# Optimization experiments

Hardware: AMD Instinct MI355X
Metric: run time of the kernel (lower is better)

The kernel has to match this reference:

```python
import jax, jax.numpy as jnp
import numpy as np

H = 10   # GRU hidden size
L = 10   # num layers
E = 400  # embedding dim
V = 100000
T, B = 84, 96


def gru_layer(x, w_ih, w_hh, b_ih, b_hh, reverse):
    # x: (T, B, in_dim); w_ih: (3H, in_dim); w_hh: (3H, H)
    xp = jnp.einsum('tbi,gi->tbg', x, w_ih) + b_ih  # (T, B, 3H)
    if reverse:
        xp = xp[::-1]

    def step(h, xt):
        gh = h @ w_hh.T + b_hh
        xr, xz, xn = jnp.split(xt, 3, axis=-1)
        hr, hz, hn = jnp.split(gh, 3, axis=-1)
        r = jax.nn.sigmoid(xr + hr)
        z = jax.nn.sigmoid(xz + hz)
        n = jnp.tanh(xn + r * hn)
        h_new = (1.0 - z) * n + z * h
        return h_new, h_new

    h0 = jnp.zeros((x.shape[1], H), x.dtype)
    _, ys = jax.lax.scan(step, h0, xp)
    if reverse:
        ys = ys[::-1]
    return ys  # (T, B, H)


def setup_inputs():
    key = jax.random.key(0)
    ks = jax.random.split(key, 12)
    s = 0.05
    return {
        'x': jax.random.randint(ks[0], (T, B), 0, V),
        'emb': jax.random.normal(ks[1], (V, E), jnp.float32) * 0.1,
        'w_ih0': jax.random.normal(ks[2], (2, 3 * H, E), jnp.float32) * s,
        'w_hh0': jax.random.normal(ks[3], (2, 3 * H, H), jnp.float32) * s,
        'b_ih0': jax.random.normal(ks[4], (2, 3 * H), jnp.float32) * s,
        'b_hh0': jax.random.normal(ks[5], (2, 3 * H), jnp.float32) * s,
        'w_ih': jax.random.normal(ks[6], (L - 1, 2, 3 * H, 2 * H), jnp.float32) * s,
        'w_hh': jax.random.normal(ks[7], (L - 1, 2, 3 * H, H), jnp.float32) * s,
        'b_ih': jax.random.normal(ks[8], (L - 1, 2, 3 * H), jnp.float32) * s,
        'b_hh': jax.random.normal(ks[9], (L - 1, 2, 3 * H), jnp.float32) * s,
        'lin_w': jax.random.normal(ks[10], (19, 336), jnp.float32) * s,
        'lin_b': jax.random.normal(ks[11], (19,), jnp.float32) * s,
    }


def reference(x, emb, w_ih0, w_hh0, b_ih0, b_hh0, w_ih, w_hh, b_ih, b_hh, lin_w, lin_b):
    out = emb[x]  # (T, B, 400)
    for l in range(L):
        if l == 0:
            wi, wh, bi, bh = w_ih0, w_hh0, b_ih0, b_hh0
        else:
            wi, wh, bi, bh = w_ih[l - 1], w_hh[l - 1], b_ih[l - 1], b_hh[l - 1]
        fwd = gru_layer(out, wi[0], wh[0], bi[0], bh[0], False)
        bwd = gru_layer(out, wi[1], wh[1], bi[1], bh[1], True)
        out = jnp.concatenate([fwd, bwd], axis=-1)  # (T, B, 20)
        # dropout p=0.2 between layers is disabled (eval-mode reference)
    # AvgPool2d(3)/MaxPool2d(3) on 3D input pool over (batch, feature) dims
    trimmed = out[:, : (B // 3) * 3, :18].reshape(T, B // 3, 3, 6, 3)
    avg = trimmed.mean(axis=(2, 4))  # (T, B//3, 6)
    mx = trimmed.max(axis=(2, 4))    # (T, B//3, 6)
    cat = jnp.concatenate([avg, mx], axis=2)  # (T, B//3, 12)
    flat = cat.reshape(-1, 336)  # (96, 336)
    # dropout p=0.2 disabled (eval-mode reference)
    return jax.nn.sigmoid(flat @ lin_w.T + lin_b)
```

## Files before the change

### kernel.cpp

```cpp
#include <hip/hip_runtime.h>
#include <math.h>

#define TT 84
#define BB 96
#define GB 6
#define NG 16
#define NTOK (TT*BB)
#define RW4 6

#define S_RZ (-1.4426950408889634f)
#define S_N  (-2.8853900817779268f)

__device__ __forceinline__ float frcp(float x)  { return __builtin_amdgcn_rcpf(x); }
__device__ __forceinline__ float fexp2(float x) { return __builtin_amdgcn_exp2f(x); }

__global__ __launch_bounds__(256) void proj0_kernel(
    const int* __restrict__ x, const float* __restrict__ emb,
    const float* __restrict__ wih0, const float* __restrict__ bih0,
    float* __restrict__ xp, unsigned int* __restrict__ bar)
{
    if (blockIdx.x == 0 && threadIdx.x == 0) bar[0] = 0u;
    __shared__ float4 xrow[32][100];
    const int tok0 = blockIdx.x * 32;
    for (int u = threadIdx.x; u < 32*100; u += 256) {
        int tk = u / 100, i4 = u % 100;
        int row = x[tok0 + tk];
        xrow[tk][i4] = ((const float4*)emb)[row*100 + i4];
    }
    __syncthreads();
    const int g64 = threadIdx.x & 63;
    const int q   = threadIdx.x >> 6;
    if (g64 >= 60) return;
    const int dir = g64 / 30, gg = g64 % 30;
    const float sc = (gg < 20) ? S_RZ : S_N;
    const float bias = bih0[dir*30 + gg];
    float acc[8];
    #pragma unroll
    for (int c = 0; c < 8; ++c) acc[c] = bias;
    const float4* w4 = ((const float4*)wih0) + (dir*30 + gg)*100;
    for (int i4 = 0; i4 < 100; ++i4) {
        float4 w = w4[i4];
        #pragma unroll
        for (int c = 0; c < 8; ++c) {
            float4 xv = xrow[q*8 + c][i4];
            acc[c] += w.x*xv.x + w.y*xv.y + w.z*xv.z + w.w*xv.w;
        }
    }
    #pragma unroll
    for (int c = 0; c < 8; ++c) {
        int tok = tok0 + q*8 + c;
        int t = tok / BB, b = tok % BB;
        xp[((size_t)((dir*TT + t)*BB + b))*30 + gg] = acc[c]*sc;
    }
}

__device__ __forceinline__ float gru_cell10(
    float xr, float xz, float xn, const float* h,
    const float* wr, const float* wz, const float* wn,
    float bhr, float bhz, float bhn, float& hown)
{
    float hr0 = fmaf(wr[0], h[0], bhr), hr1 = wr[1]*h[1];
    float hz0 = fmaf(wz[0], h[0], bhz), hz1 = wz[1]*h[1];
    float hn0 = fmaf(wn[0], h[0], bhn), hn1 = wn[1]*h[1];
    hr0 = fmaf(wr[2], h[2], hr0); hr1 = fmaf(wr[3], h[3], hr1);
    hz0 = fmaf(wz[2], h[2], hz0); hz1 = fmaf(wz[3], h[3], hz1);
    hn0 = fmaf(wn[2], h[2], hn0); hn1 = fmaf(wn[3], h[3], hn1);
    hr0 = fmaf(wr[4], h[4], hr0); hr1 = fmaf(wr[5], h[5], hr1);
    hz0 = fmaf(wz[4], h[4], hz0); hz1 = fmaf(wz[5], h[5], hz1);
    hn0 = fmaf(wn[4], h[4], hn0); hn1 = fmaf(wn[5], h[5], hn1);
    hr0 = fmaf(wr[6], h[6], hr0); hr1 = fmaf(wr[7], h[7], hr1);
    hz0 = fmaf(wz[6], h[6], hz0); hz1 = fmaf(wz[7], h[7], hz1);
    hn0 = fmaf(wn[6], h[6], hn0); hn1 = fmaf(wn[7], h[7], hn1);
    hr0 = fmaf(wr[8], h[8], hr0); hr1 = fmaf(wr[9], h[9], hr1);
    hz0 = fmaf(wz[8], h[8], hz0); hz1 = fmaf(wz[9], h[9], hz1);
    hn0 = fmaf(wn[8], h[8], hn0); hn1 = fmaf(wn[9], h[9], hn1);
    float r = frcp(1.f + fexp2(xr + hr0 + hr1));
    float z = frcp(1.f + fexp2(xz + hz0 + hz1));
    float an = fmaf(r, hn0 + hn1, xn);
    float n  = fmaf(2.f, frcp(1.f + fexp2(an)), -1.f);
    float hnew = n + z*(hown - n);
    hown = hnew;
    return hnew;
}

__device__ __forceinline__ void proj20(
    const float4* A, const float* wpr, const float* wpz, const float* wpn,
    float bir, float biz, float bin, float& xr, float& xz, float& xn)
{
    float a[24];
    #pragma unroll
    for (int q = 0; q < 6; ++q) {
        a[4*q]=A[q].x; a[4*q+1]=A[q].y; a[4*q+2]=A[q].z; a[4*q+3]=A[q].w;
    }
    xr = bir; xz = biz; xn = bin;
    #pragma unroll
    for (int c = 0; c < 20; ++c) {
        float av = a[c + (c >= 10 ? 2 : 0)];
        xr = fmaf(wpr[c], av, xr); xz = fmaf(wpz[c], av, xz); xn = fmaf(wpn[c], av, xn);
    }
}

__device__ __forceinline__ void scan_layer(
    const float* __restrict__ xb,
    const float* __restrict__ wh, const float* __restrict__ bh3,
    float4* __restrict__ act4, float* __restrict__ actG, bool last,
    int bl, int j, bool act_ln, int b, int dir, int dt, int t0)
{
    float wr[10], wz[10], wn[10];
    {
        const float2* p0 = (const float2*)(wh + j*10);
        const float2* p1 = (const float2*)(wh + (10+j)*10);
        const float2* p2 = (const float2*)(wh + (20+j)*10);
        #pragma unroll
        for (int q = 0; q < 5; ++q) {
            float2 a = p0[q]; wr[2*q]=a.x*S_RZ; wr[2*q+1]=a.y*S_RZ;
            float2 c = p1[q]; wz[2*q]=c.x*S_RZ; wz[2*q+1]=c.y*S_RZ;
            float2 d = p2[q]; wn[2*q]=d.x*S_N;  wn[2*q+1]=d.y*S_N;
        }
    }
    const float bhr = bh3[j]*S_RZ, bhz = bh3[10+j]*S_RZ, bhn = bh3[20+j]*S_N;

    const int base = bl*10;
    float h[10];
    #pragma unroll
    for (int k = 0; k < 10; ++k) h[k] = 0.f;
    float hown = 0.f;
    int t = t0;
    float xr0 = xb[(size_t)(t0*BB + b)*30 + j];
    float xz0 = xb[(size_t)(t0*BB + b)*30 + 10 + j];
    float xn0 = xb[(size_t)(t0*BB + b)*30 + 20 + j];
    const int t1 = t0 + dt;
    float xr1 = xb[(size_t)(t1*BB + b)*30 + j];
    float xz1 = xb[(size_t)(t1*BB + b)*30 + 10 + j];
    float xn1 = xb[(size_t)(t1*BB + b)*30 + 20 + j];

    #pragma unroll 1
    for (int s = 0; s < TT; ++s) {
        float hnew = gru_cell10(xr0, xz0, xn0, h, wr, wz, wn, bhr, bhz, bhn, hown);
        #pragma unroll
        for (int k = 0; k < 10; ++k) h[k] = __shfl(hnew, base + k, 64);
        if (!last) {
            ((float*)&act4[(t*GB + bl)*RW4])[dir*12 + j] = hnew;
        } else if (act_ln) {
            actG[(size_t)(t*BB + b)*20 + dir*10 + j] = hnew;
        }
        int tp = t + 2*dt; tp = tp < 0 ? 0 : (tp > TT-1 ? TT-1 : tp);
        xr0 = xr1; xz0 = xz1; xn0 = xn1;
        const float* px = xb + (size_t)(tp*BB + b)*30;
        xr1 = px[j]; xz1 = px[10 + j]; xn1 = px[20 + j];
        t += dt;
    }
}

__global__ __launch_bounds__(256, 1) void mega_kernel(
    float* __restrict__ xp,
    const float* __restrict__ whh0, const float* __restrict__ bhh0,
    const float* __restrict__ wih,  const float* __restrict__ bih,
    const float* __restrict__ whh,  const float* __restrict__ bhh,
    const float* __restrict__ lin_w, const float* __restrict__ lin_b,
    float* __restrict__ actG, unsigned int* __restrict__ bar,
    float* __restrict__ out)
{
    __shared__ float4 act4[TT*GB*RW4];

    const int tid  = threadIdx.x;
    const int grp  = blockIdx.x;

    const int dir  = (tid >> 6) & 1;
    const int lane = tid & 63;
    int bl = lane / 10; if (bl > 5) bl = 5;
    int j  = lane - bl*10; if (j > 9) j = 9;
    const bool act_ln = (lane < 60);
    const int b  = grp*GB + bl;
    const int dt = dir ? -1 : 1;
    const int t0 = dir ? TT-1 : 0;

    const int half = tid / 120;
    const int prr  = tid % 120;
    const int dp   = prr / 60;
    const int prr2 = prr % 60;
    const int blp  = prr2 / 10;
    const int jp   = prr2 % 10;

    #pragma unroll 1
    for (int l = 0; l < 10; ++l) {
        if (tid < 128) {
            const float* wh  = (l == 0) ? (whh0 + dir*300)
                                        : (whh + (size_t)((l-1)*2 + dir)*300);
            const float* bh3 = (l == 0) ? (bhh0 + dir*30)
                                        : (bhh + (size_t)((l-1)*2 + dir)*30);
            scan_layer(xp + (size_t)dir*TT*BB*30, wh, bh3, act4, actG, (l == 9),
                       bl, j, act_ln, b, dir, dt, t0);
        }
        __syncthreads();
        if (l < 9) {
            if (tid < 240) {
                const float* wi = wih + (size_t)(l*2 + dp)*600;
                const float* bi = bih + (size_t)(l*2 + dp)*30;
                float wpr[20], wpz[20], wpn[20];
                {
                    const float4* p0 = (const float4*)(wi + jp*20);
                    const float4* p1 = (const float4*)(wi + (10+jp)*20);
                    const float4* p2 = (const float4*)(wi + (20+jp)*20);
                    #pragma unroll
                    for (int q = 0; q < 5; ++q) {
                        float4 a = p0[q]; wpr[4*q]=a.x*S_RZ; wpr[4*q+1]=a.y*S_RZ; wpr[4*q+2]=a.z*S_RZ; wpr[4*q+3]=a.w*S_RZ;
                        float4 c = p1[q]; wpz[4*q]=c.x*S_RZ; wpz[4*q+1]=c.y*S_RZ; wpz[4*q+2]=c.z*S_RZ; wpz[4*q+3]=c.w*S_RZ;
                        float4 d = p2[q]; wpn[4*q]=d.x*S_N;  wpn[4*q+1]=d.y*S_N;  wpn[4*q+2]=d.z*S_N;  wpn[4*q+3]=d.w*S_N;
                    }
                }
                const float bir = bi[jp]*S_RZ, biz = bi[10+jp]*S_RZ, bin = bi[20+jp]*S_N;
                const int bg = grp*GB + blp;
                #pragma unroll 1
                for (int t = half*(TT/2); t < (half+1)*(TT/2); ++t) {
                    float xr, xz, xn;
                    proj20(&act4[(t*GB + blp)*RW4], wpr, wpz, wpn, bir, biz, bin, xr, xz, xn);
                    float* px = xp + ((size_t)(dp*TT + t)*BB + bg)*30;
                    px[jp] = xr; px[10+jp] = xz; px[20+jp] = xn;
                }
            }
            __syncthreads();
        }
    }

    __threadfence();
    __syncthreads();
    if (tid == 0) {
        __hip_atomic_fetch_add(bar, 1u, __ATOMIC_ACQ_REL, __HIP_MEMORY_SCOPE_AGENT);
        while (__hip_atomic_load(bar, __ATOMIC_ACQUIRE, __HIP_MEMORY_SCOPE_AGENT) < (unsigned)NG)
            __builtin_amdgcn_s_sleep(1);
    }
    __syncthreads();
    __threadfence();

    float* feat = (float*)act4;
    for (int u = tid; u < GB*336; u += 256) {
        int q = u / 336, v = u % 336;
        int r = grp*GB + q;
        int qq = v / 12, f = v % 12;
        int pair = r*28 + qq;
        int t = pair / 32, bb = pair % 32;
        int jj = (f < 6) ? f : f - 6;
        float acc = (f < 6) ? 0.f : -1e30f;
        #pragma unroll
        for (int i = 0; i < 3; ++i) {
            #pragma unroll
            for (int kk = 0; kk < 3; ++kk) {
                float vv = actG[(size_t)(t*BB + bb*3 + i)*20 + jj*3 + kk];
                if (f < 6) acc += vv; else acc = fmaxf(acc, vv);
            }
        }
        feat[u] = (f < 6) ? acc*(1.f/9.f) : acc;
    }
    __syncthreads();
    if (tid < GB*19) {
        int q = tid / 19, o = tid % 19;
        int r = grp*GB + q;
        float acc = lin_b[o];
        const float* wrow = lin_w + o*336;
        const float* frow = feat + q*336;
        for (int v = 0; v < 336; ++v) acc = fmaf(frow[v], wrow[v], acc);
        out[r*19 + o] = frcp(1.f + __expf(-acc));
    }
}

extern "C" void kernel_launch(void* const* d_in, const int* in_sizes, int n_in,
                              void* d_out, int out_size, void* d_ws, size_t ws_size,
                              hipStream_t stream)
{
    const int*   x     = (const int*)  d_in[0];
    const float* emb   = (const float*)d_in[1];
    const float* wih0  = (const float*)d_in[2];
    const float* whh0  = (const float*)d_in[3];
    const float* bih0  = (const float*)d_in[4];
    const float* bhh0  = (const float*)d_in[5];
    const float* wih   = (const float*)d_in[6];
    const float* whh   = (const float*)d_in[7];
    const float* bih   = (const float*)d_in[8];
    const float* bhh   = (const float*)d_in[9];
    const float* lin_w = (const float*)d_in[10];
    const float* lin_b = (const float*)d_in[11];
    float* out = (float*)d_out;

    float* xp0  = (float*)d_ws;
    float* actG = xp0 + (size_t)2*NTOK*30;
    unsigned int* bar = (unsigned int*)(actG + (size_t)NTOK*20);

    proj0_kernel<<<252, 256, 0, stream>>>(x, emb, wih0, bih0, xp0, bar);
    mega_kernel<<<NG, 256, 0, stream>>>(xp0, whh0, bhh0, wih, bih, whh, bhh,
                                        lin_w, lin_b, actG, bar, out);
}
```

Measured before the change: 532.7 us.

## Remap GRU scan to 16-lane rows with DPP rotate broadcast of hidden state

The recurrent scan is reorganised so each sequence occupies a 16-lane DPP row, and three wavefronts now hold all 12 sequences where two did before. The ten per-step __shfl broadcasts of the hidden state are replaced by row_ror DPP moves, with the recurrent weights pre-rotated and zero-padded to 16 entries. Padding lanes write to a trash slot in shared memory instead of branching. The aim is to cut cross-lane latency on the serial critical path, at the cost of 16-wide dot products (more FMAs per step) and extra registers.

```diff
diff --git a/kernel.cpp b/kernel.cpp
--- a/kernel.cpp
+++ b/kernel.cpp
@@ -13,6 +13,12 @@
 
 __device__ __forceinline__ float frcp(float x)  { return __builtin_amdgcn_rcpf(x); }
 __device__ __forceinline__ float fexp2(float x) { return __builtin_amdgcn_exp2f(x); }
+
+template<int M>
+__device__ __forceinline__ float dpp_ror(float v) {
+    return __int_as_float(__builtin_amdgcn_update_dpp(
+        0, __float_as_int(v), 0x120 + M, 0xf, 0xf, true));
+}
 
 __global__ __launch_bounds__(256) void proj0_kernel(
     const int* __restrict__ x, const float* __restrict__ emb,
@@ -54,35 +60,6 @@
     }
 }
 
-__device__ __forceinline__ float gru_cell10(
-    float xr, float xz, float xn, const float* h,
-    const float* wr, const float* wz, const float* wn,
-    float bhr, float bhz, float bhn, float& hown)
-{
-    float hr0 = fmaf(wr[0], h[0], bhr), hr1 = wr[1]*h[1];
-    float hz0 = fmaf(wz[0], h[0], bhz), hz1 = wz[1]*h[1];
-    float hn0 = fmaf(wn[0], h[0], bhn), hn1 = wn[1]*h[1];
-    hr0 = fmaf(wr[2], h[2], hr0); hr1 = fmaf(wr[3], h[3], hr1);
-    hz0 = fmaf(wz[2], h[2], hz0); hz1 = fmaf(wz[3], h[3], hz1);
-    hn0 = fmaf(wn[2], h[2], hn0); hn1 = fmaf(wn[3], h[3], hn1);
-    hr0 = fmaf(wr[4], h[4], hr0); hr1 = fmaf(wr[5], h[5], hr1);
-    hz0 = fmaf(wz[4], h[4], hz0); hz1 = fmaf(wz[5], h[5], hz1);
-    hn0 = fmaf(wn[4], h[4], hn0); hn1 = fmaf(wn[5], h[5], hn1);
-    hr0 = fmaf(wr[6], h[6], hr0); hr1 = fmaf(wr[7], h[7], hr1);
-    hz0 = fmaf(wz[6], h[6], hz0); hz1 = fmaf(wz[7], h[7], hz1);
-    hn0 = fmaf(wn[6], h[6], hn0); hn1 = fmaf(wn[7], h[7], hn1);
-    hr0 = fmaf(wr[8], h[8], hr0); hr1 = fmaf(wr[9], h[9], hr1);
-    hz0 = fmaf(wz[8], h[8], hz0); hz1 = fmaf(wz[9], h[9], hz1);
-    hn0 = fmaf(wn[8], h[8], hn0); hn1 = fmaf(wn[9], h[9], hn1);
-    float r = frcp(1.f + fexp2(xr + hr0 + hr1));
-    float z = frcp(1.f + fexp2(xz + hz0 + hz1));
-    float an = fmaf(r, hn0 + hn1, xn);
-    float n  = fmaf(2.f, frcp(1.f + fexp2(an)), -1.f);
-    float hnew = n + z*(hown - n);
-    hown = hnew;
-    return hnew;
-}
-
 __device__ __forceinline__ void proj20(
     const float4* A, const float* wpr, const float* wpz, const float* wpn,
     float bir, float biz, float bin, float& xr, float& xz, float& xn)
@@ -100,54 +77,86 @@
     }
 }
 
-__device__ __forceinline__ void scan_layer(
+template<bool LAST>
+__device__ __forceinline__ void scan16(
     const float* __restrict__ xb,
     const float* __restrict__ wh, const float* __restrict__ bh3,
-    float4* __restrict__ act4, float* __restrict__ actG, bool last,
-    int bl, int j, bool act_ln, int b, int dir, int dt, int t0)
-{
-    float wr[10], wz[10], wn[10];
-    {
-        const float2* p0 = (const float2*)(wh + j*10);
-        const float2* p1 = (const float2*)(wh + (10+j)*10);
-        const float2* p2 = (const float2*)(wh + (20+j)*10);
-        #pragma unroll
-        for (int q = 0; q < 5; ++q) {
-            float2 a = p0[q]; wr[2*q]=a.x*S_RZ; wr[2*q+1]=a.y*S_RZ;
-            float2 c = p1[q]; wz[2*q]=c.x*S_RZ; wz[2*q+1]=c.y*S_RZ;
-            float2 d = p2[q]; wn[2*q]=d.x*S_N;  wn[2*q+1]=d.y*S_N;
-        }
-    }
-    const float bhr = bh3[j]*S_RZ, bhz = bh3[10+j]*S_RZ, bhn = bh3[20+j]*S_N;
-
-    const int base = bl*10;
-    float h[10];
-    #pragma unroll
-    for (int k = 0; k < 10; ++k) h[k] = 0.f;
-    float hown = 0.f;
+    float* __restrict__ actF, float* __restrict__ actG,
+    int j, int jw, int bl, int dir, int b, int dt, int t0,
+    bool realw, int trashIdx)
+{
+    float wsr[16], wsz[16], wsn[16];
+    #pragma unroll
+    for (int m = 0; m < 16; ++m) {
+        int k  = (j - m) & 15;
+        int kc = (k < 10) ? k : 9;
+        float zr = (k < 10) ? S_RZ : 0.f;
+        float zn = (k < 10) ? S_N  : 0.f;
+        wsr[m] = wh[       jw*10 + kc] * zr;
+        wsz[m] = wh[100 +  jw*10 + kc] * zr;
+        wsn[m] = wh[200 +  jw*10 + kc] * zn;
+    }
+    const float bhr = bh3[jw]*S_RZ, bhz = bh3[10+jw]*S_RZ, bhn = bh3[20+jw]*S_N;
+
+    float h[16];
+    #pragma unroll
+    for (int m = 0; m < 16; ++m) h[m] = 0.f;
+
     int t = t0;
-    float xr0 = xb[(size_t)(t0*BB + b)*30 + j];
-    float xz0 = xb[(size_t)(t0*BB + b)*30 + 10 + j];
-    float xn0 = xb[(size_t)(t0*BB + b)*30 + 20 + j];
+    const size_t lbo = (size_t)b*30 + jw;
+    float xr0 = xb[(size_t)t0*(BB*30) + lbo];
+    float xz0 = xb[(size_t)t0*(BB*30) + lbo + 10];
+    float xn0 = xb[(size_t)t0*(BB*30) + lbo + 20];
     const int t1 = t0 + dt;
-    float xr1 = xb[(size_t)(t1*BB + b)*30 + j];
-    float xz1 = xb[(size_t)(t1*BB + b)*30 + 10 + j];
-    float xn1 = xb[(size_t)(t1*BB + b)*30 + 20 + j];
+    float xr1 = xb[(size_t)t1*(BB*30) + lbo];
+    float xz1 = xb[(size_t)t1*(BB*30) + lbo + 10];
+    float xn1 = xb[(size_t)t1*(BB*30) + lbo + 20];
 
     #pragma unroll 1
     for (int s = 0; s < TT; ++s) {
-        float hnew = gru_cell10(xr0, xz0, xn0, h, wr, wz, wn, bhr, bhz, bhn, hown);
+        float ar0 = fmaf(wsr[0], h[0], xr0 + bhr), ar1 = wsr[1]*h[1];
+        float az0 = fmaf(wsz[0], h[0], xz0 + bhz), az1 = wsz[1]*h[1];
+        float an0 = fmaf(wsn[0], h[0], bhn),       an1 = wsn[1]*h[1];
         #pragma unroll
-        for (int k = 0; k < 10; ++k) h[k] = __shfl(hnew, base + k, 64);
-        if (!last) {
-            ((float*)&act4[(t*GB + bl)*RW4])[dir*12 + j] = hnew;
-        } else if (act_ln) {
-            actG[(size_t)(t*BB + b)*20 + dir*10 + j] = hnew;
-        }
+        for (int m = 2; m < 16; m += 2) {
+            ar0 = fmaf(wsr[m], h[m], ar0); ar1 = fmaf(wsr[m+1], h[m+1], ar1);
+            az0 = fmaf(wsz[m], h[m], az0); az1 = fmaf(wsz[m+1], h[m+1], az1);
+            an0 = fmaf(wsn[m], h[m], an0); an1 = fmaf(wsn[m+1], h[m+1], an1);
+        }
+        float r  = frcp(1.f + fexp2(ar0 + ar1));
+        float z  = frcp(1.f + fexp2(az0 + az1));
+        float an = fmaf(r, an0 + an1, xn0);
+        float n  = fmaf(2.f, frcp(1.f + fexp2(an)), -1.f);
+        float hown = h[0];
+        float hnew = n + z*(hown - n);
+
+        int widx = realw ? ((t*GB + bl)*24 + dir*12 + j) : trashIdx;
+        actF[widx] = hnew;
+        if (LAST) {
+            if (realw) actG[(size_t)(t*BB + b)*20 + dir*10 + j] = hnew;
+        }
+
+        h[0]  = hnew;
+        h[1]  = dpp_ror<1>(hnew);
+        h[2]  = dpp_ror<2>(hnew);
+        h[3]  = dpp_ror<3>(hnew);
+        h[4]  = dpp_ror<4>(hnew);
+        h[5]  = dpp_ror<5>(hnew);
+        h[6]  = dpp_ror<6>(hnew);
+        h[7]  = dpp_ror<7>(hnew);
+        h[8]  = dpp_ror<8>(hnew);
+        h[9]  = dpp_ror<9>(hnew);
+        h[10] = dpp_ror<10>(hnew);
+        h[11] = dpp_ror<11>(hnew);
+        h[12] = dpp_ror<12>(hnew);
+        h[13] = dpp_ror<13>(hnew);
+        h[14] = dpp_ror<14>(hnew);
+        h[15] = dpp_ror<15>(hnew);
+
         int tp = t + 2*dt; tp = tp < 0 ? 0 : (tp > TT-1 ? TT-1 : tp);
         xr0 = xr1; xz0 = xz1; xn0 = xn1;
-        const float* px = xb + (size_t)(tp*BB + b)*30;
-        xr1 = px[j]; xz1 = px[10 + j]; xn1 = px[20 + j];
+        const float* px = xb + (size_t)tp*(BB*30) + lbo;
+        xr1 = px[0]; xz1 = px[10]; xn1 = px[20];
         t += dt;
     }
 }
@@ -161,19 +170,25 @@
     float* __restrict__ actG, unsigned int* __restrict__ bar,
     float* __restrict__ out)
 {
-    __shared__ float4 act4[TT*GB*RW4];
+    __shared__ float4 act4[TT*GB*RW4 + 16];
 
     const int tid  = threadIdx.x;
     const int grp  = blockIdx.x;
-
-    const int dir  = (tid >> 6) & 1;
+    const int wid  = tid >> 6;
     const int lane = tid & 63;
-    int bl = lane / 10; if (bl > 5) bl = 5;
-    int j  = lane - bl*10; if (j > 9) j = 9;
-    const bool act_ln = (lane < 60);
-    const int b  = grp*GB + bl;
-    const int dt = dir ? -1 : 1;
-    const int t0 = dir ? TT-1 : 0;
+
+    const bool scanw = (wid < 3);
+    const int seq  = wid*4 + (lane >> 4);
+    const int rl   = lane & 15;
+    const int dirS = (seq >= 6) ? 1 : 0;
+    const int blS  = seq - dirS*6;
+    const int jS   = rl;
+    const int jwS  = (rl < 10) ? rl : 9;
+    const bool realw = (rl < 10);
+    const int bS   = grp*GB + blS;
+    const int dtS  = dirS ? -1 : 1;
+    const int t0S  = dirS ? TT-1 : 0;
+    const int trashIdx = TT*GB*RW4*4 + lane;
 
     const int half = tid / 120;
     const int prr  = tid % 120;
@@ -183,44 +198,50 @@
     const int jp   = prr2 % 10;
 
     #pragma unroll 1
-    for (int l = 0; l < 10; ++l) {
-        if (tid < 128) {
-            const float* wh  = (l == 0) ? (whh0 + dir*300)
-                                        : (whh + (size_t)((l-1)*2 + dir)*300);
-            const float* bh3 = (l == 0) ? (bhh0 + dir*30)
-                                        : (bhh + (size_t)((l-1)*2 + dir)*30);
-            scan_layer(xp + (size_t)dir*TT*BB*30, wh, bh3, act4, actG, (l == 9),
-                       bl, j, act_ln, b, dir, dt, t0);
+    for (int l = 0; l < 9; ++l) {
+        if (scanw) {
+            const float* wh  = (l == 0) ? (whh0 + dirS*300)
+                                        : (whh + (size_t)((l-1)*2 + dirS)*300);
+            const float* bh3 = (l == 0) ? (bhh0 + dirS*30)
+                                        : (bhh + (size_t)((l-1)*2 + dirS)*30);
+            scan16<false>(xp + (size_t)dirS*TT*BB*30, wh, bh3,
+                          (float*)act4, actG, jS, jwS, blS, dirS, bS, dtS, t0S,
+                          realw, trashIdx);
         }
         __syncthreads();
-        if (l < 9) {
-            if (tid < 240) {
-                const float* wi = wih + (size_t)(l*2 + dp)*600;
-                const float* bi = bih + (size_t)(l*2 + dp)*30;
-                float wpr[20], wpz[20], wpn[20];
-                {
-                    const float4* p0 = (const float4*)(wi + jp*20);
-                    const float4* p1 = (const float4*)(wi + (10+jp)*20);
-                    const float4* p2 = (const float4*)(wi + (20+jp)*20);
-                    #pragma unroll
-                    for (int q = 0; q < 5; ++q) {
-                        float4 a = p0[q]; wpr[4*q]=a.x*S_RZ; wpr[4*q+1]=a.y*S_RZ; wpr[4*q+2]=a.z*S_RZ; wpr[4*q+3]=a.w*S_RZ;
-                        float4 c = p1[q]; wpz[4*q]=c.x*S_RZ; wpz[4*q+1]=c.y*S_RZ; wpz[4*q+2]=c.z*S_RZ; wpz[4*q+3]=c.w*S_RZ;
-                        float4 d = p2[q]; wpn[4*q]=d.x*S_N;  wpn[4*q+1]=d.y*S_N;  wpn[4*q+2]=d.z*S_N;  wpn[4*q+3]=d.w*S_N;
-                    }
-                }
-                const float bir = bi[jp]*S_RZ, biz = bi[10+jp]*S_RZ, bin = bi[20+jp]*S_N;
-                const int bg = grp*GB + blp;
-                #pragma unroll 1
-                for (int t = half*(TT/2); t < (half+1)*(TT/2); ++t) {
-                    float xr, xz, xn;
-                    proj20(&act4[(t*GB + blp)*RW4], wpr, wpz, wpn, bir, biz, bin, xr, xz, xn);
-                    float* px = xp + ((size_t)(dp*TT + t)*BB + bg)*30;
-                    px[jp] = xr; px[10+jp] = xz; px[20+jp] = xn;
+        if (tid < 240) {
+            const float* wi = wih + (size_t)(l*2 + dp)*600;
+            const float* bi = bih + (size_t)(l*2 + dp)*30;
+            float wpr[20], wpz[20], wpn[20];
+            {
+                const float4* p0 = (const float4*)(wi + jp*20);
+                const float4* p1 = (const float4*)(wi + (10+jp)*20);
+                const float4* p2 = (const float4*)(wi + (20+jp)*20);
+                #pragma unroll
+                for (int q = 0; q < 5; ++q) {
+                    float4 a = p0[q]; wpr[4*q]=a.x*S_RZ; wpr[4*q+1]=a.y*S_RZ; wpr[4*q+2]=a.z*S_RZ; wpr[4*q+3]=a.w*S_RZ;
+                    float4 c = p1[q]; wpz[4*q]=c.x*S_RZ; wpz[4*q+1]=c.y*S_RZ; wpz[4*q+2]=c.z*S_RZ; wpz[4*q+3]=c.w*S_RZ;
+                    float4 d = p2[q]; wpn[4*q]=d.x*S_N;  wpn[4*q+1]=d.y*S_N;  wpn[4*q+2]=d.z*S_N;  wpn[4*q+3]=d.w*S_N;
                 }
             }
-            __syncthreads();
-        }
+            const float bir = bi[jp]*S_RZ, biz = bi[10+jp]*S_RZ, bin = bi[20+jp]*S_N;
+            const int bg = grp*GB + blp;
+            #pragma unroll 1
+            for (int t = half*(TT/2); t < (half+1)*(TT/2); ++t) {
+                float xr, xz, xn;
+                proj20(&act4[(t*GB + blp)*RW4], wpr, wpz, wpn, bir, biz, bin, xr, xz, xn);
+                float* px = xp + ((size_t)(dp*TT + t)*BB + bg)*30;
+                px[jp] = xr; px[10+jp] = xz; px[20+jp] = xn;
+            }
+        }
+        __syncthreads();
+    }
+    if (scanw) {
+        const float* wh  = whh + (size_t)(8*2 + dirS)*300;
+        const float* bh3 = bhh + (size_t)(8*2 + dirS)*30;
+        scan16<true>(xp + (size_t)dirS*TT*BB*30, wh, bh3,
+                     (float*)act4, actG, jS, jwS, blS, dirS, bS, dtS, t0S,
+                     realw, trashIdx);
     }
 
     __threadfence();
```

Result: no change. 534.6 us (+0.3%).
